# Performance work log

Hardware: AMD Instinct MI355X
Metric: run time of the kernel (lower is better)

## Reference

```python
import jax, jax.numpy as jnp
import numpy as np

N = 100000      # nodes
E = 3200000     # edges (avg degree 32)
NFEAT = 512
HID = 64
NCLASS = 64
ALPHA = 0.1
NITER = 10


def setup_inputs() -> dict:
    key = jax.random.key(0)
    k1, k2, k3, k4, k5 = jax.random.split(key, 5)
    x = jax.random.normal(k1, (N, NFEAT), dtype=jnp.float32)
    edge_index = jax.random.randint(k2, (2, E), 0, N, dtype=jnp.int32)
    edge_weight = jax.random.uniform(k3, (E,), dtype=jnp.float32)
    W1 = jax.random.normal(k4, (NFEAT, HID), dtype=jnp.float32) * 0.05
    W2 = jax.random.normal(k5, (HID, NCLASS), dtype=jnp.float32) * 0.05
    return {"x": x, "edge_index": edge_index, "edge_weight": edge_weight,
            "W1": W1, "W2": W2}


def reference(x, edge_index, edge_weight, W1, W2):
    # _transform_features (eval mode: dropout = identity, bias=False)
    h = jax.nn.relu(x @ W1)            # [N, HID]
    z0 = h @ W2                        # [N, NCLASS]
    src = edge_index[0]
    dst = edge_index[1]
    z = z0
    # APPNP power iteration: z = adj @ z + alpha * z0
    for _ in range(NITER):
        msg = edge_weight[:, None] * z[src]                          # [E, NCLASS]
        z = jax.ops.segment_sum(msg, dst, num_segments=N) + ALPHA * z0
    return jax.nn.log_softmax(z, axis=-1)
```

## Files before the change

kernel.cpp:

```cpp
#include <hip/hip_runtime.h>

#define NN     100000
#define EE     3200000
#define NF     512
#define HIDN   64
#define NCLS   64
#define ALPHA  0.1f

#define CHUNK  512
#define NB     196

template <bool RELU, bool DUP>
__global__ __launch_bounds__(256) void gemm_kernel(
    const float* __restrict__ A, const float* __restrict__ B,
    float* __restrict__ C, float* __restrict__ C2, int nrows, int K)
{
    const int BK = 16;
    __shared__ float AsT[BK][68];
    __shared__ float Bs [BK][68];

    int tid = threadIdx.x;
    int tx  = tid & 15;
    int ty  = tid >> 4;
    int rowBase = blockIdx.x * 64;

    int arow = tid >> 2;
    int ak   = (tid & 3) * 4;
    int brow = tid >> 4;
    int bcol = (tid & 15) * 4;

    float acc[4][4] = {};

    for (int k0 = 0; k0 < K; k0 += BK) {
        float4 av;
        int gr = rowBase + arow;
        if (gr < nrows) av = *(const float4*)(A + (size_t)gr * K + k0 + ak);
        else            av = make_float4(0.f, 0.f, 0.f, 0.f);
        float4 bv = *(const float4*)(B + (size_t)(k0 + brow) * 64 + bcol);

        __syncthreads();
        AsT[ak + 0][arow] = av.x;
        AsT[ak + 1][arow] = av.y;
        AsT[ak + 2][arow] = av.z;
        AsT[ak + 3][arow] = av.w;
        *(float4*)&Bs[brow][bcol] = bv;
        __syncthreads();

#pragma unroll
        for (int kk = 0; kk < BK; ++kk) {
            float4 a = *(const float4*)&AsT[kk][ty * 4];
            float4 b = *(const float4*)&Bs [kk][tx * 4];
            acc[0][0] = fmaf(a.x, b.x, acc[0][0]);
            acc[0][1] = fmaf(a.x, b.y, acc[0][1]);
            acc[0][2] = fmaf(a.x, b.z, acc[0][2]);
            acc[0][3] = fmaf(a.x, b.w, acc[0][3]);
            acc[1][0] = fmaf(a.y, b.x, acc[1][0]);
            acc[1][1] = fmaf(a.y, b.y, acc[1][1]);
            acc[1][2] = fmaf(a.y, b.z, acc[1][2]);
            acc[1][3] = fmaf(a.y, b.w, acc[1][3]);
            acc[2][0] = fmaf(a.z, b.x, acc[2][0]);
            acc[2][1] = fmaf(a.z, b.y, acc[2][1]);
            acc[2][2] = fmaf(a.z, b.z, acc[2][2]);
            acc[2][3] = fmaf(a.z, b.w, acc[2][3]);
            acc[3][0] = fmaf(a.w, b.x, acc[3][0]);
            acc[3][1] = fmaf(a.w, b.y, acc[3][1]);
            acc[3][2] = fmaf(a.w, b.z, acc[3][2]);
            acc[3][3] = fmaf(a.w, b.w, acc[3][3]);
        }
    }

#pragma unroll
    for (int i = 0; i < 4; ++i) {
        int r = rowBase + ty * 4 + i;
        if (r < nrows) {
            float4 o;
            o.x = acc[i][0]; o.y = acc[i][1]; o.z = acc[i][2]; o.w = acc[i][3];
            if (RELU) {
                o.x = fmaxf(o.x, 0.f); o.y = fmaxf(o.y, 0.f);
                o.z = fmaxf(o.z, 0.f); o.w = fmaxf(o.w, 0.f);
            }
            *(float4*)(C + (size_t)r * 64 + tx * 4) = o;
            if (DUP) *(float4*)(C2 + (size_t)r * 64 + tx * 4) = o;
        }
    }
}

__global__ __launch_bounds__(256) void zero_kernel(int* __restrict__ p, int n)
{
    int i = blockIdx.x * 256 + threadIdx.x;
    if (i < n) p[i] = 0;
}

__global__ __launch_bounds__(256) void count_kernel(const int* __restrict__ dst,
                                                    int* __restrict__ deg)
{
    int e = blockIdx.x * 256 + threadIdx.x;
    if (e < EE) atomicAdd(&deg[dst[e]], 1);
}

__global__ __launch_bounds__(256) void scanA_kernel(const int* __restrict__ deg,
                                                    int* __restrict__ bsum)
{
    int b = blockIdx.x, t = threadIdx.x;
    int i = b * CHUNK + t * 2;
    int v = 0;
    if (i < NN)     v += deg[i];
    if (i + 1 < NN) v += deg[i + 1];
    __shared__ int sm[256];
    sm[t] = v;
    __syncthreads();
    for (int o = 128; o > 0; o >>= 1) {
        if (t < o) sm[t] += sm[t + o];
        __syncthreads();
    }
    if (t == 0) bsum[b] = sm[0];
}

__global__ __launch_bounds__(256) void scanB_kernel(const int* __restrict__ bsum,
                                                    int* __restrict__ bbase,
                                                    int* __restrict__ offs)
{
    int t = threadIdx.x;
    int v = (t < NB) ? bsum[t] : 0;
    __shared__ int sm[256];
    sm[t] = v;
    __syncthreads();
    for (int o = 1; o < 256; o <<= 1) {
        int u = (t >= o) ? sm[t - o] : 0;
        __syncthreads();
        sm[t] += u;
        __syncthreads();
    }
    if (t < NB) bbase[t] = sm[t] - v;
    if (t == 0) offs[NN] = EE;
}

__global__ __launch_bounds__(256) void scanC_kernel(const int* __restrict__ deg,
                                                    const int* __restrict__ bbase,
                                                    int* __restrict__ offs,
                                                    int* __restrict__ cursor)
{
    int b = blockIdx.x, t = threadIdx.x;
    int i0 = b * CHUNK + t * 2;
    int d0 = (i0 < NN)     ? deg[i0]     : 0;
    int d1 = (i0 + 1 < NN) ? deg[i0 + 1] : 0;
    int local = d0 + d1;
    __shared__ int sm[256];
    sm[t] = local;
    __syncthreads();
    for (int o = 1; o < 256; o <<= 1) {
        int u = (t >= o) ? sm[t - o] : 0;
        __syncthreads();
        sm[t] += u;
        __syncthreads();
    }
    int excl = sm[t] - local + bbase[b];
    if (i0 < NN)     { offs[i0]     = excl;      cursor[i0]     = excl;      }
    if (i0 + 1 < NN) { offs[i0 + 1] = excl + d0; cursor[i0 + 1] = excl + d0; }
}

__global__ __launch_bounds__(256) void scatter_kernel(
    const int* __restrict__ src, const int* __restrict__ dst,
    const float* __restrict__ w, int* cursor, int2* __restrict__ csr)
{
    int e = blockIdx.x * 256 + threadIdx.x;
    if (e >= EE) return;
    int d = dst[e];
    int pos = atomicAdd(&cursor[d], 1);
    csr[pos] = make_int2(src[e], __float_as_int(w[e]));
}

template <bool LSM>
__global__ __launch_bounds__(256) void propagate_kernel(
    const float* __restrict__ zin, const float* __restrict__ z0,
    float* __restrict__ zout, const int* __restrict__ offs,
    const int2* __restrict__ csr)
{
    int gid  = blockIdx.x * 256 + threadIdx.x;
    int node = gid >> 6;
    int lane = gid & 63;
    if (node >= NN) return;

    int beg = offs[node];
    int end = offs[node + 1];
    float acc = 0.f;
    int j = beg;
    for (; j + 4 <= end; j += 4) {
        int2 e0 = csr[j],     e1 = csr[j + 1];
        int2 e2 = csr[j + 2], e3 = csr[j + 3];
        float v0 = zin[(size_t)e0.x * 64 + lane];
        float v1 = zin[(size_t)e1.x * 64 + lane];
        float v2 = zin[(size_t)e2.x * 64 + lane];
        float v3 = zin[(size_t)e3.x * 64 + lane];
        acc = fmaf(__int_as_float(e0.y), v0, acc);
        acc = fmaf(__int_as_float(e1.y), v1, acc);
        acc = fmaf(__int_as_float(e2.y), v2, acc);
        acc = fmaf(__int_as_float(e3.y), v3, acc);
    }
    for (; j < end; ++j) {
        int2 e = csr[j];
        acc = fmaf(__int_as_float(e.y), zin[(size_t)e.x * 64 + lane], acc);
    }

    float out = fmaf(ALPHA, z0[(size_t)node * 64 + lane], acc);

    if (LSM) {
        float m = out;
#pragma unroll
        for (int o = 32; o > 0; o >>= 1) m = fmaxf(m, __shfl_xor(m, o, 64));
        float e = __expf(out - m);
        float s = e;
#pragma unroll
        for (int o = 32; o > 0; o >>= 1) s += __shfl_xor(s, o, 64);
        out = (out - m) - __logf(s);
    }
    zout[(size_t)node * 64 + lane] = out;
}

extern "C" void kernel_launch(void* const* d_in, const int* in_sizes, int n_in,
                              void* d_out, int out_size, void* d_ws, size_t ws_size,
                              hipStream_t stream)
{
    const float* x  = (const float*)d_in[0];
    const int*   ei = (const int*)  d_in[1];
    const float* ew = (const float*)d_in[2];
    const float* W1 = (const float*)d_in[3];
    const float* W2 = (const float*)d_in[4];
    const int* src = ei;
    const int* dst = ei + EE;

    char* ws = (char*)d_ws;
    size_t off = 0;
    auto alloc = [&](size_t bytes) -> char* {
        char* p = ws + off;
        off += (bytes + 255) & ~(size_t)255;
        return p;
    };

    float* h     = (float*)alloc((size_t)NN * HIDN * 4);
    float* z0    = (float*)alloc((size_t)NN * NCLS * 4);
    float* zB    = (float*)alloc((size_t)NN * NCLS * 4);
    int*   deg   = (int*)  alloc((size_t)NN * 4);
    int*   offs  = (int*)  alloc((size_t)(NN + 1) * 4);
    int*   cur_  = (int*)  alloc((size_t)NN * 4);
    int*   bsum  = (int*)  alloc((size_t)NB * 4);
    int*   bbase = (int*)  alloc((size_t)NB * 4);

    int2* csr = (int2*)h;
    float* zA = (float*)d_out;

    gemm_kernel<true, false><<<(NN + 63) / 64, 256, 0, stream>>>(x, W1, h, nullptr, NN, NF);
    gemm_kernel<false, true><<<(NN + 63) / 64, 256, 0, stream>>>(h, W2, z0, zA, NN, HIDN);

    zero_kernel<<<(NN + 255) / 256, 256, 0, stream>>>(deg, NN);
    count_kernel<<<EE / 256, 256, 0, stream>>>(dst, deg);
    scanA_kernel<<<NB, 256, 0, stream>>>(deg, bsum);
    scanB_kernel<<<1, 256, 0, stream>>>(bsum, bbase, offs);
    scanC_kernel<<<NB, 256, 0, stream>>>(deg, bbase, offs, cur_);
    scatter_kernel<<<EE / 256, 256, 0, stream>>>(src, dst, ew, cur_, csr);

    const float* cur = zA;
    float* nxt = zB;
    for (int it = 0; it < 10; ++it) {
        if (it < 9)
            propagate_kernel<false><<<(NN * 64) / 256, 256, 0, stream>>>(cur, z0, nxt, offs, csr);
        else
            propagate_kernel<true ><<<(NN * 64) / 256, 256, 0, stream>>>(cur, z0, nxt, offs, csr);
        float* t = (float*)cur; cur = nxt; nxt = t;
    }
}
```

Baseline: 1.846 ms.

## Store propagated features in bf16 and build CSR via bucketed two-pass scatter

The APPNP iteration state is now stored in bf16, halving the bytes gathered per edge in each propagation step, while accumulation stays in fp32 and the final step writes fp32 log-softmax. CSR construction is split into a coarse bucket scatter followed by a per-bucket placement, improving write locality of the atomic scatter. The gather loop is unrolled to 8 edges. This trades numerical precision for memory traffic and adds extra kernels.

Measured after the change: 2.291 ms. 24.1% more time.

```diff
diff --git a/kernel.cpp b/kernel.cpp
--- a/kernel.cpp
+++ b/kernel.cpp
@@ -10,10 +10,27 @@
 #define CHUNK  512
 #define NB     196
 
-template <bool RELU, bool DUP>
+#define BSHIFT 7
+#define NBUCK  782
+
+typedef unsigned short ushort_t;
+typedef unsigned int   uint_t;
+
+__device__ inline ushort_t f2bf(float f)
+{
+    uint_t u = __float_as_uint(f);
+    u += 0x7FFFu + ((u >> 16) & 1u);
+    return (ushort_t)(u >> 16);
+}
+__device__ inline float bf2f(ushort_t b)
+{
+    return __uint_as_float(((uint_t)b) << 16);
+}
+
+template <bool RELU>
 __global__ __launch_bounds__(256) void gemm_kernel(
     const float* __restrict__ A, const float* __restrict__ B,
-    float* __restrict__ C, float* __restrict__ C2, int nrows, int K)
+    float* __restrict__ C, int nrows, int K)
 {
     const int BK = 16;
     __shared__ float AsT[BK][68];
@@ -80,7 +97,6 @@
                 o.z = fmaxf(o.z, 0.f); o.w = fmaxf(o.w, 0.f);
             }
             *(float4*)(C + (size_t)r * 64 + tx * 4) = o;
-            if (DUP) *(float4*)(C2 + (size_t)r * 64 + tx * 4) = o;
         }
     }
 }
@@ -159,22 +175,62 @@
     if (i0 + 1 < NN) { offs[i0 + 1] = excl + d0; cursor[i0 + 1] = excl + d0; }
 }
 
-__global__ __launch_bounds__(256) void scatter_kernel(
+__global__ __launch_bounds__(256) void bcur_kernel(const int* __restrict__ offs,
+                                                   int* __restrict__ bcur)
+{
+    int b = blockIdx.x * 256 + threadIdx.x;
+    if (b < NBUCK) {
+        int n = b << BSHIFT;
+        bcur[b] = offs[n < NN ? n : NN];
+    }
+}
+
+__global__ __launch_bounds__(256) void bucketize_kernel(
     const int* __restrict__ src, const int* __restrict__ dst,
-    const float* __restrict__ w, int* cursor, int2* __restrict__ csr)
+    const float* __restrict__ w, int* bcur, int2* __restrict__ tA)
 {
     int e = blockIdx.x * 256 + threadIdx.x;
     if (e >= EE) return;
     int d = dst[e];
-    int pos = atomicAdd(&cursor[d], 1);
-    csr[pos] = make_int2(src[e], __float_as_int(w[e]));
+    int b = d >> BSHIFT;
+    int pos = atomicAdd(&bcur[b], 1);
+    tA[pos] = make_int2(src[e] | ((d & ((1 << BSHIFT) - 1)) << 17),
+                        __float_as_int(w[e]));
+}
+
+__global__ __launch_bounds__(256) void place_kernel(
+    const int2* __restrict__ tA, const int* __restrict__ offs,
+    int* cursor, int2* __restrict__ csr)
+{
+    int b  = blockIdx.x;
+    int n0 = b << BSHIFT;
+    int n1 = (b + 1) << BSHIFT; if (n1 > NN) n1 = NN;
+    int base = offs[n0];
+    int end  = offs[n1];
+    for (int i = base + threadIdx.x; i < end; i += 256) {
+        int2 e = tA[i];
+        int d = n0 + (e.x >> 17);
+        int pos = atomicAdd(&cursor[d], 1);
+        csr[pos] = make_int2(e.x & 0x1FFFF, e.y);
+    }
+}
+
+__global__ __launch_bounds__(256) void cvt_kernel(const float* __restrict__ z0,
+                                                  ushort_t* __restrict__ zb)
+{
+    int i = (blockIdx.x * 256 + threadIdx.x) * 4;
+    if (i >= NN * 64) return;
+    float4 v = *(const float4*)(z0 + i);
+    ushort4 o;
+    o.x = f2bf(v.x); o.y = f2bf(v.y); o.z = f2bf(v.z); o.w = f2bf(v.w);
+    *(ushort4*)(zb + i) = o;
 }
 
 template <bool LSM>
 __global__ __launch_bounds__(256) void propagate_kernel(
-    const float* __restrict__ zin, const float* __restrict__ z0,
-    float* __restrict__ zout, const int* __restrict__ offs,
-    const int2* __restrict__ csr)
+    const ushort_t* __restrict__ zin, const float* __restrict__ z0,
+    ushort_t* __restrict__ zout_b, float* __restrict__ zout_f,
+    const int* __restrict__ offs, const int2* __restrict__ csr)
 {
     int gid  = blockIdx.x * 256 + threadIdx.x;
     int node = gid >> 6;
@@ -185,21 +241,29 @@
     int end = offs[node + 1];
     float acc = 0.f;
     int j = beg;
-    for (; j + 4 <= end; j += 4) {
-        int2 e0 = csr[j],     e1 = csr[j + 1];
-        int2 e2 = csr[j + 2], e3 = csr[j + 3];
-        float v0 = zin[(size_t)e0.x * 64 + lane];
-        float v1 = zin[(size_t)e1.x * 64 + lane];
-        float v2 = zin[(size_t)e2.x * 64 + lane];
-        float v3 = zin[(size_t)e3.x * 64 + lane];
+    for (; j + 8 <= end; j += 8) {
+        int2 e0 = csr[j],     e1 = csr[j + 1], e2 = csr[j + 2], e3 = csr[j + 3];
+        int2 e4 = csr[j + 4], e5 = csr[j + 5], e6 = csr[j + 6], e7 = csr[j + 7];
+        float v0 = bf2f(zin[(size_t)e0.x * 64 + lane]);
+        float v1 = bf2f(zin[(size_t)e1.x * 64 + lane]);
+        float v2 = bf2f(zin[(size_t)e2.x * 64 + lane]);
+        float v3 = bf2f(zin[(size_t)e3.x * 64 + lane]);
+        float v4 = bf2f(zin[(size_t)e4.x * 64 + lane]);
+        float v5 = bf2f(zin[(size_t)e5.x * 64 + lane]);
+        float v6 = bf2f(zin[(size_t)e6.x * 64 + lane]);
+        float v7 = bf2f(zin[(size_t)e7.x * 64 + lane]);
         acc = fmaf(__int_as_float(e0.y), v0, acc);
         acc = fmaf(__int_as_float(e1.y), v1, acc);
         acc = fmaf(__int_as_float(e2.y), v2, acc);
         acc = fmaf(__int_as_float(e3.y), v3, acc);
+        acc = fmaf(__int_as_float(e4.y), v4, acc);
+        acc = fmaf(__int_as_float(e5.y), v5, acc);
+        acc = fmaf(__int_as_float(e6.y), v6, acc);
+        acc = fmaf(__int_as_float(e7.y), v7, acc);
     }
     for (; j < end; ++j) {
         int2 e = csr[j];
-        acc = fmaf(__int_as_float(e.y), zin[(size_t)e.x * 64 + lane], acc);
+        acc = fmaf(__int_as_float(e.y), bf2f(zin[(size_t)e.x * 64 + lane]), acc);
     }
 
     float out = fmaf(ALPHA, z0[(size_t)node * 64 + lane], acc);
@@ -212,9 +276,10 @@
         float s = e;
 #pragma unroll
         for (int o = 32; o > 0; o >>= 1) s += __shfl_xor(s, o, 64);
-        out = (out - m) - __logf(s);
-    }
-    zout[(size_t)node * 64 + lane] = out;
+        zout_f[(size_t)node * 64 + lane] = (out - m) - __logf(s);
+    } else {
+        zout_b[(size_t)node * 64 + lane] = f2bf(out);
+    }
 }
 
 extern "C" void kernel_launch(void* const* d_in, const int* in_sizes, int n_in,
@@ -237,35 +302,41 @@
         return p;
     };
 
-    float* h     = (float*)alloc((size_t)NN * HIDN * 4);
-    float* z0    = (float*)alloc((size_t)NN * NCLS * 4);
-    float* zB    = (float*)alloc((size_t)NN * NCLS * 4);
-    int*   deg   = (int*)  alloc((size_t)NN * 4);
-    int*   offs  = (int*)  alloc((size_t)(NN + 1) * 4);
-    int*   cur_  = (int*)  alloc((size_t)NN * 4);
-    int*   bsum  = (int*)  alloc((size_t)NB * 4);
-    int*   bbase = (int*)  alloc((size_t)NB * 4);
+    float*    h     = (float*)   alloc((size_t)NN * HIDN * 4);
+    float*    z0    = (float*)   alloc((size_t)NN * NCLS * 4);
+    ushort_t* zbA   = (ushort_t*)alloc((size_t)NN * NCLS * 2);
+    ushort_t* zbB   = (ushort_t*)alloc((size_t)NN * NCLS * 2);
+    int*      deg   = (int*)     alloc((size_t)NN * 4);
+    int*      offs  = (int*)     alloc((size_t)(NN + 1) * 4);
+    int*      cur_  = (int*)     alloc((size_t)NN * 4);
+    int*      bsum  = (int*)     alloc((size_t)NB * 4);
+    int*      bbase = (int*)     alloc((size_t)NB * 4);
+    int*      bcur  = (int*)     alloc((size_t)NBUCK * 4);
 
     int2* csr = (int2*)h;
-    float* zA = (float*)d_out;
-
-    gemm_kernel<true, false><<<(NN + 63) / 64, 256, 0, stream>>>(x, W1, h, nullptr, NN, NF);
-    gemm_kernel<false, true><<<(NN + 63) / 64, 256, 0, stream>>>(h, W2, z0, zA, NN, HIDN);
+    int2* tA  = (int2*)zbA;
+
+    gemm_kernel<true ><<<(NN + 63) / 64, 256, 0, stream>>>(x, W1, h, NN, NF);
+    gemm_kernel<false><<<(NN + 63) / 64, 256, 0, stream>>>(h, W2, z0, NN, HIDN);
 
     zero_kernel<<<(NN + 255) / 256, 256, 0, stream>>>(deg, NN);
     count_kernel<<<EE / 256, 256, 0, stream>>>(dst, deg);
     scanA_kernel<<<NB, 256, 0, stream>>>(deg, bsum);
     scanB_kernel<<<1, 256, 0, stream>>>(bsum, bbase, offs);
     scanC_kernel<<<NB, 256, 0, stream>>>(deg, bbase, offs, cur_);
-    scatter_kernel<<<EE / 256, 256, 0, stream>>>(src, dst, ew, cur_, csr);
-
-    const float* cur = zA;
-    float* nxt = zB;
-    for (int it = 0; it < 10; ++it) {
-        if (it < 9)
-            propagate_kernel<false><<<(NN * 64) / 256, 256, 0, stream>>>(cur, z0, nxt, offs, csr);
-        else
-            propagate_kernel<true ><<<(NN * 64) / 256, 256, 0, stream>>>(cur, z0, nxt, offs, csr);
-        float* t = (float*)cur; cur = nxt; nxt = t;
-    }
-}
+    bcur_kernel<<<(NBUCK + 255) / 256, 256, 0, stream>>>(offs, bcur);
+    bucketize_kernel<<<EE / 256, 256, 0, stream>>>(src, dst, ew, bcur, tA);
+    place_kernel<<<NBUCK, 256, 0, stream>>>(tA, offs, cur_, csr);
+
+    cvt_kernel<<<(NN * 64 / 4 + 255) / 256, 256, 0, stream>>>(z0, zbA);
+
+    const ushort_t* cur = zbA;
+    ushort_t* nxt = zbB;
+    for (int it = 0; it < 9; ++it) {
+        propagate_kernel<false><<<(NN * 64) / 256, 256, 0, stream>>>(
+            cur, z0, nxt, nullptr, offs, csr);
+        ushort_t* t = (ushort_t*)cur; cur = nxt; nxt = t;
+    }
+    propagate_kernel<true><<<(NN * 64) / 256, 256, 0, stream>>>(
+        cur, z0, nullptr, (float*)d_out, offs, csr);
+}
```
